# Kernel optimization log

Hardware: AMD Instinct MI355X
Metric: run time of the kernel (lower is better)

## Reference

```python
import jax, jax.numpy as jnp
import numpy as np

N = 100000
E = 1600000
F_IN = 128
HID = 64
HEADS = 2
OUT_HEADS = 1
NUM_CLASS = 18
NEG_SLOPE = 0.2


def setup_inputs() -> dict:
    key = jax.random.key(0)
    ks = jax.random.split(key, 12)
    x = jax.random.normal(ks[0], (N, F_IN), dtype=jnp.float32)
    edge_index = jax.random.randint(ks[1], (2, E), 0, N, dtype=jnp.int64)
    s = lambda k, shp, fan: jax.random.normal(k, shp, dtype=jnp.float32) * (1.0 / np.sqrt(fan))
    W0 = s(ks[2], (F_IN, HID), F_IN)
    b0 = jnp.zeros((HID,), dtype=jnp.float32)
    W1 = s(ks[3], (HID, HEADS * HID), HID)
    att_src1 = s(ks[4], (HEADS, HID), HID)
    att_dst1 = s(ks[5], (HEADS, HID), HID)
    b1 = jnp.zeros((HEADS * HID,), dtype=jnp.float32)
    W2 = s(ks[6], (HEADS * HID, OUT_HEADS * NUM_CLASS), HEADS * HID)
    att_src2 = s(ks[7], (OUT_HEADS, NUM_CLASS), NUM_CLASS)
    att_dst2 = s(ks[8], (OUT_HEADS, NUM_CLASS), NUM_CLASS)
    b2 = jnp.zeros((OUT_HEADS * NUM_CLASS,), dtype=jnp.float32)
    return {"x": x, "edge_index": edge_index, "W0": W0, "b0": b0,
            "W1": W1, "att_src1": att_src1, "att_dst1": att_dst1, "b1": b1,
            "W2": W2, "att_src2": att_src2, "att_dst2": att_dst2, "b2": b2}


def gat_conv(x, src, dst, W, att_s, att_d, bias, heads, out_ch):
    n = x.shape[0]
    h = (x @ W).reshape(n, heads, out_ch)              # [N,H,C]
    a_s = jnp.sum(h * att_s, axis=-1)                   # [N,H]
    a_d = jnp.sum(h * att_d, axis=-1)                   # [N,H]
    e = jax.nn.leaky_relu(a_s[src] + a_d[dst], NEG_SLOPE)  # [E,H]
    m = jax.ops.segment_max(e, dst, num_segments=n)
    ex = jnp.exp(e - m[dst])
    denom = jax.ops.segment_sum(ex, dst, num_segments=n)
    alpha = ex / denom[dst]                              # [E,H]
    msg = h[src] * alpha[:, :, None]                     # [E,H,C]
    out = jax.ops.segment_sum(msg, dst, num_segments=n)  # [N,H,C]
    return out.reshape(n, heads * out_ch) + bias


def reference(x, edge_index, W0, b0, W1, att_src1, att_dst1, b1, W2, att_src2, att_dst2, b2):
    n = x.shape[0]
    # PyG GATConv adds self-loops by default
    loops = jnp.arange(n, dtype=edge_index.dtype)
    src = jnp.concatenate([edge_index[0], loops])
    dst = jnp.concatenate([edge_index[1], loops])
    # eval mode: dropout is identity
    h = jax.nn.relu(x @ W0 + b0)
    h = jax.nn.elu(gat_conv(h, src, dst, W1, att_src1, att_dst1, b1, HEADS, HID))
    out = gat_conv(h, src, dst, W2, att_src2, att_dst2, b2, OUT_HEADS, NUM_CLASS)
    return jax.nn.log_softmax(out, axis=-1)
```

## Files before the change

### kernel.cpp

```cpp
#include <hip/hip_runtime.h>
#include <math.h>


#define NEG_SLOPE 0.2f
#define STASH_CAP 128

typedef unsigned short ushort_t;

__device__ __forceinline__ float wmax(float v) {
    for (int o = 32; o; o >>= 1) v = fmaxf(v, __shfl_xor(v, o));
    return v;
}
__device__ __forceinline__ float wsum(float v) {
    for (int o = 32; o; o >>= 1) v += __shfl_xor(v, o);
    return v;
}

__device__ __forceinline__ unsigned bfpack(float a, float b) {
    unsigned ua = __float_as_uint(a);
    unsigned ub = __float_as_uint(b);
    ua = (ua + 0x7fffu + ((ua >> 16) & 1u)) >> 16;
    ub = (ub + 0x7fffu + ((ub >> 16) & 1u)) & 0xffff0000u;
    return ua | ub;
}
__device__ __forceinline__ ushort_t bf16of(float a) {
    unsigned ua = __float_as_uint(a);
    return (ushort_t)((ua + 0x7fffu + ((ua >> 16) & 1u)) >> 16);
}
__device__ __forceinline__ float bflo(unsigned u) { return __uint_as_float(u << 16); }
__device__ __forceinline__ float bfhi(unsigned u) { return __uint_as_float(u & 0xffff0000u); }
__device__ __forceinline__ float bfval(ushort_t u) { return __uint_as_float(((unsigned)u) << 16); }

__global__ void k_deg_init(int* __restrict__ deg, int N) {
    int i = blockIdx.x * blockDim.x + threadIdx.x;
    if (i < N) deg[i] = 1;
}
__global__ void k_deg_edges(const int* __restrict__ ei, int* __restrict__ deg,
                            int* __restrict__ eofs, int E) {
    int e = blockIdx.x * blockDim.x + threadIdx.x;
    if (e < E) eofs[e] = atomicAdd(&deg[ei[E + e]], 1);
}

__global__ __launch_bounds__(256) void k_scan1(const int* __restrict__ deg, int* __restrict__ rs,
                                               int* __restrict__ bsum, int N) {
    __shared__ int s[256];
    int t = threadIdx.x;
    int base = blockIdx.x * 1024;
    int i0 = base + t * 4;
    int d0 = (i0 + 0 < N) ? deg[i0 + 0] : 0;
    int d1 = (i0 + 1 < N) ? deg[i0 + 1] : 0;
    int d2 = (i0 + 2 < N) ? deg[i0 + 2] : 0;
    int d3 = (i0 + 3 < N) ? deg[i0 + 3] : 0;
    int s0 = d0, s1 = s0 + d1, s2 = s1 + d2, s3 = s2 + d3;
    int tsum = s3;
    s[t] = tsum;
    __syncthreads();
    for (int off = 1; off < 256; off <<= 1) {
        int v = (t >= off) ? s[t - off] : 0;
        __syncthreads();
        s[t] += v;
        __syncthreads();
    }
    int excl = s[t] - tsum;
    if (i0 + 0 < N) rs[1 + i0 + 0] = excl + s0;
    if (i0 + 1 < N) rs[1 + i0 + 1] = excl + s1;
    if (i0 + 2 < N) rs[1 + i0 + 2] = excl + s2;
    if (i0 + 3 < N) rs[1 + i0 + 3] = excl + s3;
    if (t == 0) bsum[blockIdx.x] = s[255];
}

__global__ __launch_bounds__(256) void k_scan2(const int* __restrict__ bsum,
                                               int* __restrict__ boff, int NB) {
    __shared__ int s[256];
    int t = threadIdx.x;
    int orig = (t < NB) ? bsum[t] : 0;
    s[t] = orig;
    __syncthreads();
    for (int off = 1; off < 256; off <<= 1) {
        int v = (t >= off) ? s[t - off] : 0;
        __syncthreads();
        s[t] += v;
        __syncthreads();
    }
    if (t < NB) boff[t] = s[t] - orig;
}

__global__ void k_scan3(int* __restrict__ rs, const int* __restrict__ boff, int N) {
    int i = blockIdx.x * blockDim.x + threadIdx.x;
    if (i == 0) rs[0] = 0;
    if (i < N) rs[1 + i] += boff[i >> 10];
}

__global__ __launch_bounds__(256) void k_scatter(const int* __restrict__ ei,
                                                 const int* __restrict__ eofs,
                                                 const int* __restrict__ rs,
                                                 int* __restrict__ csr,
                                                 int E, int Etot, int cohortBlocks) {
    int c = blockIdx.x & 7;
    int pb = blockIdx.x >> 3;
    int tid = pb * 256 + threadIdx.x;
    int stride = cohortBlocks * 256;
    for (int e = tid; e < Etot; e += stride) {
        int dst = (e < E) ? ei[E + e] : (e - E);
        if (((dst >> 13) & 7) != c) continue;
        int src, ofs;
        if (e < E) { src = ei[e]; ofs = eofs[e]; } else { src = dst; ofs = 0; }
        csr[rs[dst] + ofs] = src;
    }
}


__global__ __launch_bounds__(256) void k_gemm1(const float* __restrict__ x,
                                               const float* __restrict__ W0,
                                               const float* __restrict__ b0,
                                               unsigned* __restrict__ h0b, int N) {
    __shared__ float wl[128 * 64];
    __shared__ float al[64 * 132];
    int t = threadIdx.x;
    int n0 = blockIdx.x * 64;
    const float4* wg = (const float4*)W0;
    float4* wl4 = (float4*)wl;
#pragma unroll
    for (int i = 0; i < 8; ++i) wl4[t + i * 256] = wg[t + i * 256];
#pragma unroll
    for (int i = 0; i < 8; ++i) {
        int f = t + i * 256;
        int node = f >> 5, q = f & 31;
        int ng = n0 + node; if (ng > N - 1) ng = N - 1;
        float4 v = ((const float4*)x)[(size_t)ng * 32 + q];
        *(float4*)&al[node * 132 + q * 4] = v;
    }
    __syncthreads();
    int colg = t & 15;
    int rowg = t >> 4;
    float4 acc[4];
#pragma unroll
    for (int j = 0; j < 4; ++j) acc[j] = make_float4(0.f, 0.f, 0.f, 0.f);
    for (int k4 = 0; k4 < 128; k4 += 4) {
        float4 w0 = *(float4*)&wl[(k4 + 0) * 64 + colg * 4];
        float4 w1 = *(float4*)&wl[(k4 + 1) * 64 + colg * 4];
        float4 w2 = *(float4*)&wl[(k4 + 2) * 64 + colg * 4];
        float4 w3 = *(float4*)&wl[(k4 + 3) * 64 + colg * 4];
#pragma unroll
        for (int j = 0; j < 4; ++j) {
            float4 a = *(float4*)&al[(rowg * 4 + j) * 132 + k4];
            acc[j].x += a.x * w0.x + a.y * w1.x + a.z * w2.x + a.w * w3.x;
            acc[j].y += a.x * w0.y + a.y * w1.y + a.z * w2.y + a.w * w3.y;
            acc[j].z += a.x * w0.z + a.y * w1.z + a.z * w2.z + a.w * w3.z;
            acc[j].w += a.x * w0.w + a.y * w1.w + a.z * w2.w + a.w * w3.w;
        }
    }
    float4 bb = ((const float4*)b0)[colg];
#pragma unroll
    for (int j = 0; j < 4; ++j) {
        int n = n0 + rowg * 4 + j;
        if (n < N) {
            float rx = fmaxf(acc[j].x + bb.x, 0.f);
            float ry = fmaxf(acc[j].y + bb.y, 0.f);
            float rz = fmaxf(acc[j].z + bb.z, 0.f);
            float rw = fmaxf(acc[j].w + bb.w, 0.f);
            uint2 pr; pr.x = bfpack(rx, ry); pr.y = bfpack(rz, rw);
            ((uint2*)h0b)[(size_t)n * 16 + colg] = pr;
        }
    }
}

__global__ __launch_bounds__(256) void k_gemm2(const unsigned* __restrict__ h0b,
                                               const float* __restrict__ W1,
                                               const float* __restrict__ as_g,
                                               const float* __restrict__ ad_g,
                                               ushort_t* __restrict__ h1b,
                                               float* __restrict__ as1,
                                               float* __restrict__ ad1, int N) {
    __shared__ float wl[64 * 128];
    __shared__ float al[64 * 68];
    int t = threadIdx.x;
    int n0 = blockIdx.x * 64;
    const float4* wg = (const float4*)W1;
    float4* wl4 = (float4*)wl;
#pragma unroll
    for (int i = 0; i < 8; ++i) wl4[t + i * 256] = wg[t + i * 256];
#pragma unroll
    for (int i = 0; i < 2; ++i) {
        int f = t + i * 256;
        int node = f >> 3, q = f & 7;
        int ng = n0 + node; if (ng > N - 1) ng = N - 1;
        uint4 u = ((const uint4*)h0b)[(size_t)ng * 8 + q];
        float* dst = &al[node * 68 + q * 8];
        dst[0] = bflo(u.x); dst[1] = bfhi(u.x);
        dst[2] = bflo(u.y); dst[3] = bfhi(u.y);
        dst[4] = bflo(u.z); dst[5] = bfhi(u.z);
        dst[6] = bflo(u.w); dst[7] = bfhi(u.w);
    }
    __syncthreads();
    int colg = t & 31;
    int rowg = t >> 5;
    float4 acc[8];
#pragma unroll
    for (int j = 0; j < 8; ++j) acc[j] = make_float4(0.f, 0.f, 0.f, 0.f);
    for (int k4 = 0; k4 < 64; k4 += 4) {
        float4 w0 = *(float4*)&wl[(k4 + 0) * 128 + colg * 4];
        float4 w1 = *(float4*)&wl[(k4 + 1) * 128 + colg * 4];
        float4 w2 = *(float4*)&wl[(k4 + 2) * 128 + colg * 4];
        float4 w3 = *(float4*)&wl[(k4 + 3) * 128 + colg * 4];
#pragma unroll
        for (int j = 0; j < 8; ++j) {
            float4 a = *(float4*)&al[(rowg * 8 + j) * 68 + k4];
            acc[j].x += a.x * w0.x + a.y * w1.x + a.z * w2.x + a.w * w3.x;
            acc[j].y += a.x * w0.y + a.y * w1.y + a.z * w2.y + a.w * w3.y;
            acc[j].z += a.x * w0.z + a.y * w1.z + a.z * w2.z + a.w * w3.z;
            acc[j].w += a.x * w0.w + a.y * w1.w + a.z * w2.w + a.w * w3.w;
        }
    }
    float4 asv = ((const float4*)as_g)[colg];
    float4 adv = ((const float4*)ad_g)[colg];
    float ps[8], pd[8];
#pragma unroll
    for (int j = 0; j < 8; ++j) {
        ps[j] = acc[j].x * asv.x + acc[j].y * asv.y + acc[j].z * asv.z + acc[j].w * asv.w;
        pd[j] = acc[j].x * adv.x + acc[j].y * adv.y + acc[j].z * adv.z + acc[j].w * adv.w;
    }
    for (int o = 1; o < 16; o <<= 1) {
#pragma unroll
        for (int j = 0; j < 8; ++j) {
            ps[j] += __shfl_xor(ps[j], o);
            pd[j] += __shfl_xor(pd[j], o);
        }
    }
#pragma unroll
    for (int j = 0; j < 8; ++j) {
        int n = n0 + rowg * 8 + j;
        if (n < N) {
            uint2 pr;
            pr.x = bfpack(acc[j].x, acc[j].y);
            pr.y = bfpack(acc[j].z, acc[j].w);
            ((uint2*)h1b)[(size_t)n * 32 + colg] = pr;
        }
    }
    int lane = t & 63;
    if ((lane & 15) == 0) {
        int head = (lane >> 4) & 1;
#pragma unroll
        for (int j = 0; j < 8; ++j) {
            int n = n0 + rowg * 8 + j;
            if (n < N) {
                as1[n * 2 + head] = ps[j];
                ad1[n * 2 + head] = pd[j];
            }
        }
    }
}

__global__ __launch_bounds__(256) void k_node_l1(const int* __restrict__ rs,
                                                 const int* __restrict__ csr,
                                                 const ushort_t* __restrict__ h1b,
                                                 const float* __restrict__ as1,
                                                 const float* __restrict__ ad1,
                                                 const float* __restrict__ b1,
                                                 unsigned* __restrict__ aggb, int N) {
    __shared__ float4 stashE[4][STASH_CAP];
    __shared__ float2 stashA[4][128];
    int wid = threadIdx.x >> 6;
    int lane = threadIdx.x & 63;
    int n = (blockIdx.x * 256 + threadIdx.x) >> 6;
    if (n >= N) return;
    int row = rs[n], end = rs[n + 1];
    float2 adv = ((const float2*)ad1)[n];
    const float2* asp = (const float2*)as1;
    const unsigned* h1u = (const unsigned*)h1b;
    float m0 = -INFINITY, m1 = -INFINITY, l0 = 0.f, l1 = 0.f;
    for (int base = row; base < end; base += 64) {
        int idx = base + lane;
        bool act = idx < end;
        int src = act ? csr[idx] : 0;
        float2 av = asp[src];
        float e0 = av.x + adv.x, e1 = av.y + adv.y;
        e0 = e0 > 0.f ? e0 : NEG_SLOPE * e0;
        e1 = e1 > 0.f ? e1 : NEG_SLOPE * e1;
        int sidx = idx - row;
        if (act && sidx < STASH_CAP)
            stashE[wid][sidx] = make_float4(__int_as_float(src), e0, e1, 0.f);
        if (!act) { e0 = -INFINITY; e1 = -INFINITY; }
        float m0n = fmaxf(m0, wmax(e0));
        float m1n = fmaxf(m1, wmax(e1));
        float p0 = act ? __expf(e0 - m0n) : 0.f;
        float p1 = act ? __expf(e1 - m1n) : 0.f;
        l0 = l0 * __expf(m0 - m0n) + wsum(p0);
        l1 = l1 * __expf(m1 - m1n) + wsum(p1);
        m0 = m0n; m1 = m1n;
    }
    float inv0 = __builtin_amdgcn_rcpf(l0);
    float inv1 = __builtin_amdgcn_rcpf(l1);
    bool head1 = lane >= 32;
    float accx = 0.f, accy = 0.f;
    const float2* sp = &stashA[wid][head1 ? 64 : 0];
    for (int base = row; base < end; base += 64) {
        int idx = base + lane;
        bool act = idx < end;
        int sidx = idx - row;
        int src; float e0, e1;
        if (sidx < STASH_CAP) {
            float4 se = stashE[wid][sidx];
            src = __float_as_int(se.x);
            e0 = se.y; e1 = se.z;
        } else {
            src = act ? csr[idx] : 0;
            float2 av = asp[src];
            e0 = av.x + adv.x; e1 = av.y + adv.y;
            e0 = e0 > 0.f ? e0 : NEG_SLOPE * e0;
            e1 = e1 > 0.f ? e1 : NEG_SLOPE * e1;
        }
        float a0 = act ? __expf(e0 - m0) * inv0 : 0.f;
        float a1 = act ? __expf(e1 - m1) * inv1 : 0.f;
        stashA[wid][lane] = make_float2(__int_as_float(src), a0);
        stashA[wid][64 + lane] = make_float2(__int_as_float(src), a1);
        int cnt = min(64, end - base);
#pragma unroll 4
        for (int j = 0; j < cnt; ++j) {
            float2 sa = sp[j];
            int sj = __float_as_int(sa.x);
            float aj = sa.y;
            unsigned u = h1u[(size_t)sj * 64 + lane];
            accx += bflo(u) * aj;
            accy += bfhi(u) * aj;
        }
    }
    float vx = accx + b1[lane * 2];
    float vy = accy + b1[lane * 2 + 1];
    vx = vx > 0.f ? vx : __expf(vx) - 1.f;
    vy = vy > 0.f ? vy : __expf(vy) - 1.f;
    aggb[(size_t)n * 64 + lane] = bfpack(vx, vy);
}

__global__ __launch_bounds__(256, 4) void k_node2(const unsigned* __restrict__ aggb,
                                                  const float* __restrict__ W2,
                                                  const float* __restrict__ as_g,
                                                  const float* __restrict__ ad_g,
                                                  ushort_t* __restrict__ h2b,
                                                  float* __restrict__ a_s,
                                                  float* __restrict__ a_d, int N) {
    __shared__ float al[64 * 132];
    __shared__ float w2t[20 * 132];
    int t = threadIdx.x;
    int n0 = blockIdx.x * 64;
#pragma unroll
    for (int i = 0; i < 4; ++i) {
        int f = t + i * 256;
        int node = f >> 4, q = f & 15;
        int ng = n0 + node; if (ng > N - 1) ng = N - 1;
        uint4 u = ((const uint4*)aggb)[(size_t)ng * 16 + q];
        float* dst = &al[node * 132 + q * 8];
        dst[0] = bflo(u.x); dst[1] = bfhi(u.x);
        dst[2] = bflo(u.y); dst[3] = bfhi(u.y);
        dst[4] = bflo(u.z); dst[5] = bfhi(u.z);
        dst[6] = bflo(u.w); dst[7] = bfhi(u.w);
    }
    for (int i = t; i < 2560; i += 256) {
        int c = i >> 7, k = i & 127;
        w2t[c * 132 + k] = (c < 18) ? W2[k * 18 + c] : 0.f;
    }
    __syncthreads();
    int node = t >> 2;
    int cq = t & 3;
    int c0 = cq * 5;
    int n = n0 + node;
    float acc[5] = {0.f, 0.f, 0.f, 0.f, 0.f};
#pragma unroll 2
    for (int k4 = 0; k4 < 128; k4 += 4) {
        float4 a = *(float4*)&al[node * 132 + k4];
#pragma unroll
        for (int i = 0; i < 5; ++i) {
            float4 w = *(float4*)&w2t[(c0 + i) * 132 + k4];
            acc[i] += a.x * w.x + a.y * w.y + a.z * w.z + a.w * w.w;
        }
    }
    float ps = 0.f, pd = 0.f;
#pragma unroll
    for (int i = 0; i < 5; ++i) {
        int c = c0 + i;
        float asv = (c < 18) ? as_g[c] : 0.f;
        float adv = (c < 18) ? ad_g[c] : 0.f;
        ps += acc[i] * asv;
        pd += acc[i] * adv;
    }
    ps += __shfl_xor(ps, 1); ps += __shfl_xor(ps, 2);
    pd += __shfl_xor(pd, 1); pd += __shfl_xor(pd, 2);
    if (n < N) {
#pragma unroll
        for (int i = 0; i < 5; ++i) {
            int c = c0 + i;
            if (c < 18) h2b[(size_t)n * 24 + c] = bf16of(acc[i]);
        }
        if (cq == 0) { a_s[n] = ps; a_d[n] = pd; }
    }
}

__global__ __launch_bounds__(256) void k_node_l2(const int* __restrict__ rs,
                                                 const int* __restrict__ csr,
                                                 const ushort_t* __restrict__ h2b,
                                                 const float* __restrict__ as2,
                                                 const float* __restrict__ ad2,
                                                 const float* __restrict__ b2,
                                                 float* __restrict__ out, int N) {
    __shared__ float2 stash[4][STASH_CAP];
    int wid = threadIdx.x >> 6;
    int lane = threadIdx.x & 63;
    int n = (blockIdx.x * 256 + threadIdx.x) >> 6;
    if (n >= N) return;
    int row = rs[n], end = rs[n + 1];
    float adn = ad2[n];
    float m = -INFINITY, l = 0.f;
    for (int base = row; base < end; base += 64) {
        int idx = base + lane;
        bool act = idx < end;
        int src = act ? csr[idx] : 0;
        float e = as2[src] + adn;
        e = e > 0.f ? e : NEG_SLOPE * e;
        int sidx = idx - row;
        if (act && sidx < STASH_CAP)
            stash[wid][sidx] = make_float2(__int_as_float(src), e);
        if (!act) e = -INFINITY;
        float mn = fmaxf(m, wmax(e));
        float p = act ? __expf(e - mn) : 0.f;
        l = l * __expf(m - mn) + wsum(p);
        m = mn;
    }
    float invl = __builtin_amdgcn_rcpf(l);
    int g = lane / 21;
    int c = lane - g * 21;
    int cc = c < 18 ? c : 17;
    float acc = 0.f;
    int deg = end - row;
    int lim = deg < STASH_CAP ? deg : STASH_CAP;
    for (int o = g; o < lim; o += 3) {
        float2 se = stash[wid][o];
        int src = __float_as_int(se.x);
        float alpha = __expf(se.y - m) * invl;
        acc += alpha * bfval(h2b[(size_t)src * 24 + cc]);
    }
    for (int pos = row + STASH_CAP + g; pos < end; pos += 3) {
        int src = csr[pos];
        float e = as2[src] + adn;
        e = e > 0.f ? e : NEG_SLOPE * e;
        float alpha = __expf(e - m) * invl;
        acc += alpha * bfval(h2b[(size_t)src * 24 + cc]);
    }
    float t1 = __shfl(acc, (lane + 21) & 63);
    float t2 = __shfl(acc, (lane + 42) & 63);
    acc += t1 + t2;
    float bb = (lane < 18) ? b2[lane] : 0.f;
    float v = acc + bb;
    float tmx = (lane < 18) ? v : -INFINITY;
    for (int o = 16; o; o >>= 1) tmx = fmaxf(tmx, __shfl_xor(tmx, o));
    float s = (lane < 18) ? __expf(v - tmx) : 0.f;
    for (int o = 16; o; o >>= 1) s += __shfl_xor(s, o);
    float lse = tmx + __logf(s);
    if (lane < 18) out[(size_t)n * 18 + lane] = v - lse;
}

extern "C" void kernel_launch(void* const* d_in, const int* in_sizes, int n_in,
                              void* d_out, int out_size, void* d_ws, size_t ws_size,
                              hipStream_t stream) {
    const float* x      = (const float*)d_in[0];
    const int*   ei     = (const int*)d_in[1];
    const float* W0     = (const float*)d_in[2];
    const float* b0     = (const float*)d_in[3];
    const float* W1     = (const float*)d_in[4];
    const float* att_s1 = (const float*)d_in[5];
    const float* att_d1 = (const float*)d_in[6];
    const float* b1     = (const float*)d_in[7];
    const float* W2     = (const float*)d_in[8];
    const float* att_s2 = (const float*)d_in[9];
    const float* att_d2 = (const float*)d_in[10];
    const float* b2     = (const float*)d_in[11];

    const int N = in_sizes[0] / 128;
    const int E = in_sizes[1] / 2;
    const int Etot = E + N;
    const int NB = (N + 1023) / 1024;
    const int NBLK = (N + 63) / 64;

    char* w = (char*)d_ws;
    unsigned* h0b  = (unsigned*)w; w += (size_t)N * 64 * 2;
    ushort_t* h1b  = (ushort_t*)w; w += (size_t)N * 128 * 2;
    unsigned* aggb = (unsigned*)w; w += (size_t)N * 128 * 2;
    float* as1     = (float*)w;    w += (size_t)N * 2 * 4;
    float* ad1     = (float*)w;    w += (size_t)N * 2 * 4;
    ushort_t* h2b  = (ushort_t*)w; w += (size_t)N * 24 * 2;
    float* as2     = (float*)w;    w += (size_t)N * 4;
    float* ad2     = (float*)w;    w += (size_t)N * 4;
    int* deg       = (int*)w;      w += (size_t)N * 4;
    int* rs        = (int*)w;      w += (size_t)(N + 1) * 4;
    int* bsum      = (int*)w;      w += (size_t)256 * 4;
    int* boff      = (int*)w;      w += (size_t)256 * 4;
    int* eofs      = (int*)w;      w += (size_t)E * 4;
    int* csr       = (int*)w;      w += (size_t)Etot * 4;

    float* out = (float*)d_out;

    k_deg_init<<<(N + 255) / 256, 256, 0, stream>>>(deg, N);
    k_deg_edges<<<(E + 255) / 256, 256, 0, stream>>>(ei, deg, eofs, E);
    k_scan1<<<NB, 256, 0, stream>>>(deg, rs, bsum, N);
    k_scan2<<<1, 256, 0, stream>>>(bsum, boff, NB);
    k_scan3<<<(N + 255) / 256, 256, 0, stream>>>(rs, boff, N);
    const int cohortBlocks = 128;
    k_scatter<<<8 * cohortBlocks, 256, 0, stream>>>(ei, eofs, rs, csr, E, Etot, cohortBlocks);

    k_gemm1<<<NBLK, 256, 0, stream>>>(x, W0, b0, h0b, N);
    k_gemm2<<<NBLK, 256, 0, stream>>>(h0b, W1, att_s1, att_d1, h1b, as1, ad1, N);

    k_node_l1<<<(N * 64 + 255) / 256, 256, 0, stream>>>(rs, csr, h1b, as1, ad1, b1, aggb, N);

    k_node2<<<NBLK, 256, 0, stream>>>(aggb, W2, att_s2, att_d2, h2b, as2, ad2, N);
    k_node_l2<<<(N * 64 + 255) / 256, 256, 0, stream>>>(rs, csr, h2b, as2, ad2, b2, out, N);
}
```

Before: 449.3 us.

## Add single-pass low-degree fast path and vectorized 4-edge gather in GAT aggregation

```diff
diff --git a/kernel.cpp b/kernel.cpp
--- a/kernel.cpp
+++ b/kernel.cpp
@@ -258,78 +258,128 @@
                                                  const float* __restrict__ ad1,
                                                  const float* __restrict__ b1,
                                                  unsigned* __restrict__ aggb, int N) {
+    __shared__ float2 stashA[4][128];
     __shared__ float4 stashE[4][STASH_CAP];
-    __shared__ float2 stashA[4][128];
     int wid = threadIdx.x >> 6;
     int lane = threadIdx.x & 63;
     int n = (blockIdx.x * 256 + threadIdx.x) >> 6;
     if (n >= N) return;
     int row = rs[n], end = rs[n + 1];
+    int deg = end - row;
     float2 adv = ((const float2*)ad1)[n];
     const float2* asp = (const float2*)as1;
-    const unsigned* h1u = (const unsigned*)h1b;
-    float m0 = -INFINITY, m1 = -INFINITY, l0 = 0.f, l1 = 0.f;
-    for (int base = row; base < end; base += 64) {
-        int idx = base + lane;
-        bool act = idx < end;
-        int src = act ? csr[idx] : 0;
+    const char* h1base = (const char*)h1b;
+    int eg = lane >> 4;
+    int fl = lane & 15;
+    int head_off = (fl >= 8) ? 64 : 0;
+    int flbase = fl * 16;
+    float acc[8] = {0.f, 0.f, 0.f, 0.f, 0.f, 0.f, 0.f, 0.f};
+    float inv0, inv1;
+    if (deg <= 64) {
+        bool act = lane < deg;
+        int src = act ? csr[row + lane] : 0;
         float2 av = asp[src];
         float e0 = av.x + adv.x, e1 = av.y + adv.y;
         e0 = e0 > 0.f ? e0 : NEG_SLOPE * e0;
         e1 = e1 > 0.f ? e1 : NEG_SLOPE * e1;
-        int sidx = idx - row;
-        if (act && sidx < STASH_CAP)
-            stashE[wid][sidx] = make_float4(__int_as_float(src), e0, e1, 0.f);
         if (!act) { e0 = -INFINITY; e1 = -INFINITY; }
-        float m0n = fmaxf(m0, wmax(e0));
-        float m1n = fmaxf(m1, wmax(e1));
-        float p0 = act ? __expf(e0 - m0n) : 0.f;
-        float p1 = act ? __expf(e1 - m1n) : 0.f;
-        l0 = l0 * __expf(m0 - m0n) + wsum(p0);
-        l1 = l1 * __expf(m1 - m1n) + wsum(p1);
-        m0 = m0n; m1 = m1n;
-    }
-    float inv0 = __builtin_amdgcn_rcpf(l0);
-    float inv1 = __builtin_amdgcn_rcpf(l1);
-    bool head1 = lane >= 32;
-    float accx = 0.f, accy = 0.f;
-    const float2* sp = &stashA[wid][head1 ? 64 : 0];
-    for (int base = row; base < end; base += 64) {
-        int idx = base + lane;
-        bool act = idx < end;
-        int sidx = idx - row;
-        int src; float e0, e1;
-        if (sidx < STASH_CAP) {
-            float4 se = stashE[wid][sidx];
-            src = __float_as_int(se.x);
-            e0 = se.y; e1 = se.z;
-        } else {
-            src = act ? csr[idx] : 0;
+        float m0 = wmax(e0), m1 = wmax(e1);
+        float p0 = act ? __expf(e0 - m0) : 0.f;
+        float p1 = act ? __expf(e1 - m1) : 0.f;
+        inv0 = __builtin_amdgcn_rcpf(wsum(p0));
+        inv1 = __builtin_amdgcn_rcpf(wsum(p1));
+        stashA[wid][lane] = make_float2(__int_as_float(src), p0);
+        stashA[wid][64 + lane] = make_float2(__int_as_float(src), p1);
+        for (int j = 0; j < deg; j += 4) {
+            float2 sa = stashA[wid][head_off + j + eg];
+            int sj = __float_as_int(sa.x);
+            float aj = sa.y;
+            uint4 u = *(const uint4*)(h1base + (((unsigned)sj) << 8) + flbase);
+            acc[0] += bflo(u.x) * aj; acc[1] += bfhi(u.x) * aj;
+            acc[2] += bflo(u.y) * aj; acc[3] += bfhi(u.y) * aj;
+            acc[4] += bflo(u.z) * aj; acc[5] += bfhi(u.z) * aj;
+            acc[6] += bflo(u.w) * aj; acc[7] += bfhi(u.w) * aj;
+        }
+    } else {
+        inv0 = 1.f; inv1 = 1.f;
+        float m0 = -INFINITY, m1 = -INFINITY, l0 = 0.f, l1 = 0.f;
+        for (int base = row; base < end; base += 64) {
+            int idx = base + lane;
+            bool act = idx < end;
+            int src = act ? csr[idx] : 0;
             float2 av = asp[src];
-            e0 = av.x + adv.x; e1 = av.y + adv.y;
+            float e0 = av.x + adv.x, e1 = av.y + adv.y;
             e0 = e0 > 0.f ? e0 : NEG_SLOPE * e0;
             e1 = e1 > 0.f ? e1 : NEG_SLOPE * e1;
-        }
-        float a0 = act ? __expf(e0 - m0) * inv0 : 0.f;
-        float a1 = act ? __expf(e1 - m1) * inv1 : 0.f;
-        stashA[wid][lane] = make_float2(__int_as_float(src), a0);
-        stashA[wid][64 + lane] = make_float2(__int_as_float(src), a1);
-        int cnt = min(64, end - base);
-#pragma unroll 4
-        for (int j = 0; j < cnt; ++j) {
-            float2 sa = sp[j];
-            int sj = __float_as_int(sa.x);
-            float aj = sa.y;
-            unsigned u = h1u[(size_t)sj * 64 + lane];
-            accx += bflo(u) * aj;
-            accy += bfhi(u) * aj;
-        }
-    }
-    float vx = accx + b1[lane * 2];
-    float vy = accy + b1[lane * 2 + 1];
-    vx = vx > 0.f ? vx : __expf(vx) - 1.f;
-    vy = vy > 0.f ? vy : __expf(vy) - 1.f;
-    aggb[(size_t)n * 64 + lane] = bfpack(vx, vy);
+            int sidx = idx - row;
+            if (act && sidx < STASH_CAP)
+                stashE[wid][sidx] = make_float4(__int_as_float(src), e0, e1, 0.f);
+            if (!act) { e0 = -INFINITY; e1 = -INFINITY; }
+            float m0n = fmaxf(m0, wmax(e0));
+            float m1n = fmaxf(m1, wmax(e1));
+            float p0 = act ? __expf(e0 - m0n) : 0.f;
+            float p1 = act ? __expf(e1 - m1n) : 0.f;
+            l0 = l0 * __expf(m0 - m0n) + wsum(p0);
+            l1 = l1 * __expf(m1 - m1n) + wsum(p1);
+            m0 = m0n; m1 = m1n;
+        }
+        float r0 = __builtin_amdgcn_rcpf(l0);
+        float r1 = __builtin_amdgcn_rcpf(l1);
+        for (int base = row; base < end; base += 64) {
+            int idx = base + lane;
+            bool act = idx < end;
+            int sidx = idx - row;
+            int src; float e0, e1;
+            if (sidx < STASH_CAP) {
+                float4 se = stashE[wid][sidx];
+                src = __float_as_int(se.x);
+                e0 = se.y; e1 = se.z;
+            } else {
+                src = act ? csr[idx] : 0;
+                float2 av = asp[src];
+                e0 = av.x + adv.x; e1 = av.y + adv.y;
+                e0 = e0 > 0.f ? e0 : NEG_SLOPE * e0;
+                e1 = e1 > 0.f ? e1 : NEG_SLOPE * e1;
+            }
+            if (!act) src = 0;
+            float a0 = act ? __expf(e0 - m0) * r0 : 0.f;
+            float a1 = act ? __expf(e1 - m1) * r1 : 0.f;
+            stashA[wid][lane] = make_float2(__int_as_float(src), a0);
+            stashA[wid][64 + lane] = make_float2(__int_as_float(src), a1);
+            int cnt = min(64, end - base);
+            for (int j = 0; j < cnt; j += 4) {
+                float2 sa = stashA[wid][head_off + j + eg];
+                int sj = __float_as_int(sa.x);
+                float aj = sa.y;
+                uint4 u = *(const uint4*)(h1base + (((unsigned)sj) << 8) + flbase);
+                acc[0] += bflo(u.x) * aj; acc[1] += bfhi(u.x) * aj;
+                acc[2] += bflo(u.y) * aj; acc[3] += bfhi(u.y) * aj;
+                acc[4] += bflo(u.z) * aj; acc[5] += bfhi(u.z) * aj;
+                acc[6] += bflo(u.w) * aj; acc[7] += bfhi(u.w) * aj;
+            }
+        }
+    }
+#pragma unroll
+    for (int i = 0; i < 8; ++i) {
+        acc[i] += __shfl_xor(acc[i], 16);
+        acc[i] += __shfl_xor(acc[i], 32);
+    }
+    if (lane < 16) {
+        float inv = (lane >= 8) ? inv1 : inv0;
+        float4 ba = ((const float4*)b1)[lane * 2];
+        float4 bb4 = ((const float4*)b1)[lane * 2 + 1];
+        float v[8];
+        v[0] = acc[0] * inv + ba.x;  v[1] = acc[1] * inv + ba.y;
+        v[2] = acc[2] * inv + ba.z;  v[3] = acc[3] * inv + ba.w;
+        v[4] = acc[4] * inv + bb4.x; v[5] = acc[5] * inv + bb4.y;
+        v[6] = acc[6] * inv + bb4.z; v[7] = acc[7] * inv + bb4.w;
+#pragma unroll
+        for (int i = 0; i < 8; ++i) v[i] = v[i] > 0.f ? v[i] : __expf(v[i]) - 1.f;
+        uint4 pk;
+        pk.x = bfpack(v[0], v[1]); pk.y = bfpack(v[2], v[3]);
+        pk.z = bfpack(v[4], v[5]); pk.w = bfpack(v[6], v[7]);
+        ((uint4*)aggb)[(size_t)n * 16 + lane] = pk;
+    }
 }
 
 __global__ __launch_bounds__(256, 4) void k_node2(const unsigned* __restrict__ aggb,
@@ -408,48 +458,67 @@
     int n = (blockIdx.x * 256 + threadIdx.x) >> 6;
     if (n >= N) return;
     int row = rs[n], end = rs[n + 1];
+    int deg = end - row;
     float adn = ad2[n];
-    float m = -INFINITY, l = 0.f;
-    for (int base = row; base < end; base += 64) {
-        int idx = base + lane;
-        bool act = idx < end;
-        int src = act ? csr[idx] : 0;
-        float e = as2[src] + adn;
-        e = e > 0.f ? e : NEG_SLOPE * e;
-        int sidx = idx - row;
-        if (act && sidx < STASH_CAP)
-            stash[wid][sidx] = make_float2(__int_as_float(src), e);
-        if (!act) e = -INFINITY;
-        float mn = fmaxf(m, wmax(e));
-        float p = act ? __expf(e - mn) : 0.f;
-        l = l * __expf(m - mn) + wsum(p);
-        m = mn;
-    }
-    float invl = __builtin_amdgcn_rcpf(l);
     int g = lane / 21;
     int c = lane - g * 21;
     int cc = c < 18 ? c : 17;
     float acc = 0.f;
-    int deg = end - row;
-    int lim = deg < STASH_CAP ? deg : STASH_CAP;
-    for (int o = g; o < lim; o += 3) {
-        float2 se = stash[wid][o];
-        int src = __float_as_int(se.x);
-        float alpha = __expf(se.y - m) * invl;
-        acc += alpha * bfval(h2b[(size_t)src * 24 + cc]);
-    }
-    for (int pos = row + STASH_CAP + g; pos < end; pos += 3) {
-        int src = csr[pos];
+    float post;
+    if (deg <= 64) {
+        bool act = lane < deg;
+        int src = act ? csr[row + lane] : 0;
         float e = as2[src] + adn;
         e = e > 0.f ? e : NEG_SLOPE * e;
-        float alpha = __expf(e - m) * invl;
-        acc += alpha * bfval(h2b[(size_t)src * 24 + cc]);
+        if (!act) e = -INFINITY;
+        float m = wmax(e);
+        float p = act ? __expf(e - m) : 0.f;
+        post = __builtin_amdgcn_rcpf(wsum(p));
+        stash[wid][lane] = make_float2(__int_as_float(src), p);
+        for (int o = g; o < deg; o += 3) {
+            float2 se = stash[wid][o];
+            int src2 = __float_as_int(se.x);
+            acc += se.y * bfval(h2b[(size_t)src2 * 24 + cc]);
+        }
+    } else {
+        post = 1.f;
+        float m = -INFINITY, l = 0.f;
+        for (int base = row; base < end; base += 64) {
+            int idx = base + lane;
+            bool act = idx < end;
+            int src = act ? csr[idx] : 0;
+            float e = as2[src] + adn;
+            e = e > 0.f ? e : NEG_SLOPE * e;
+            int sidx = idx - row;
+            if (act && sidx < STASH_CAP)
+                stash[wid][sidx] = make_float2(__int_as_float(src), e);
+            if (!act) e = -INFINITY;
+            float mn = fmaxf(m, wmax(e));
+            float p = act ? __expf(e - mn) : 0.f;
+            l = l * __expf(m - mn) + wsum(p);
+            m = mn;
+        }
+        float invl = __builtin_amdgcn_rcpf(l);
+        int lim = deg < STASH_CAP ? deg : STASH_CAP;
+        for (int o = g; o < lim; o += 3) {
+            float2 se = stash[wid][o];
+            int src = __float_as_int(se.x);
+            float alpha = __expf(se.y - m) * invl;
+            acc += alpha * bfval(h2b[(size_t)src * 24 + cc]);
+        }
+        for (int pos = row + STASH_CAP + g; pos < end; pos += 3) {
+            int src = csr[pos];
+            float e = as2[src] + adn;
+            e = e > 0.f ? e : NEG_SLOPE * e;
+            float alpha = __expf(e - m) * invl;
+            acc += alpha * bfval(h2b[(size_t)src * 24 + cc]);
+        }
     }
     float t1 = __shfl(acc, (lane + 21) & 63);
     float t2 = __shfl(acc, (lane + 42) & 63);
     acc += t1 + t2;
     float bb = (lane < 18) ? b2[lane] : 0.f;
-    float v = acc + bb;
+    float v = acc * post + bb;
     float tmx = (lane < 18) ? v : -INFINITY;
     for (int o = 16; o; o >>= 1) tmx = fmaxf(tmx, __shfl_xor(tmx, o));
     float s = (lane < 18) ? __expf(v - tmx) : 0.f;
```

Result: no change. 446.8 us (-0.6%).
